# Performance work log

Hardware: AMD Instinct MI355X
Metric: run time of the kernel (lower is better)

## Reference

```python
import jax, jax.numpy as jnp
import numpy as np

N, E, F, H, OUT, PROP_STEPS, NUM_LAYERS = 50000, 800000, 64, 128, 32, 3, 2


def setup_inputs() -> dict:
    key = jax.random.key(0)
    ks = jax.random.split(key, 24)
    def lin(kw, kb, out_d, in_d):
        s = 1.0 / np.sqrt(in_d)
        w = jax.random.uniform(kw, (out_d, in_d), jnp.float32, -s, s)
        b = jax.random.uniform(kb, (out_d,), jnp.float32, -s, s)
        return w, b
    enc_w, enc_b = lin(ks[0], ks[1], 1, 2)
    ratt_w, ratt_b = lin(ks[2], ks[3], 1, F)
    iatt_w, iatt_b = lin(ks[4], ks[5], 1, F)
    rlin0_w, rlin0_b = lin(ks[6], ks[7], H, F)
    rlin1_w, rlin1_b = lin(ks[8], ks[9], H, H)
    ilin0_w, ilin0_b = lin(ks[10], ks[11], H, F)
    ilin1_w, ilin1_b = lin(ks[12], ks[13], H, H)
    out_w, out_b = lin(ks[14], ks[15], OUT, 2 * H)
    return {
        'real_feature': jax.random.normal(ks[16], (N, F), jnp.float32),
        'imag_feature': jax.random.normal(ks[17], (N, F), jnp.float32),
        'edge_entropy': jax.random.uniform(ks[18], (E,), jnp.float32),
        'edge_cluster_coefficient': jax.random.uniform(ks[19], (E,), jnp.float32),
        'edge_weight_sym': jax.random.uniform(ks[20], (E,), jnp.float32),
        'exp_weight_q': jnp.asarray(0.5, jnp.float32),
        'enc_w': enc_w, 'enc_b': enc_b,
        'ratt_w': ratt_w, 'ratt_b': ratt_b,
        'iatt_w': iatt_w, 'iatt_b': iatt_b,
        'rlin0_w': rlin0_w, 'rlin0_b': rlin0_b,
        'rlin1_w': rlin1_w, 'rlin1_b': rlin1_b,
        'ilin0_w': ilin0_w, 'ilin0_b': ilin0_b,
        'ilin1_w': ilin1_w, 'ilin1_b': ilin1_b,
        'out_w': out_w, 'out_b': out_b,
        'row': jax.random.randint(ks[21], (E,), 0, N, jnp.int32),
        'col': jax.random.randint(ks[22], (E,), 0, N, jnp.int32),
    }


def reference(real_feature, imag_feature, edge_entropy, edge_cluster_coefficient,
              edge_weight_sym, exp_weight_q, enc_w, enc_b, ratt_w, ratt_b,
              iatt_w, iatt_b, rlin0_w, rlin0_b, rlin1_w, rlin1_b,
              ilin0_w, ilin0_b, ilin1_w, ilin1_b, out_w, out_b, row, col):
    n = real_feature.shape[0]
    # structural encoding -> complex phase per edge (soft_label is None branch)
    structure_info = jnp.stack((edge_entropy, edge_cluster_coefficient), axis=1)  # [E,2]
    se = (structure_info @ enc_w.T + enc_b).reshape(-1)                            # [E]
    phase = exp_weight_q * se
    wr = edge_weight_sym * jnp.cos(phase)  # real adj values
    wi = edge_weight_sym * jnp.sin(phase)  # imag adj values

    reals, imags = [real_feature], [imag_feature]
    for _ in range(PROP_STEPS):
        xr = reals[-1][col]  # [E,F] gather once, shared by both SpMMs
        xi = imags[-1][col]
        # complex SpMM: (wr + i*wi) * (xr + i*xi)
        msg_r = wr[:, None] * xr - wi[:, None] * xi
        msg_i = wi[:, None] * xr + wr[:, None] * xi
        reals.append(jax.ops.segment_sum(msg_r, row, num_segments=n))
        imags.append(jax.ops.segment_sum(msg_i, row, num_segments=n))

    R = jnp.stack(reals)  # [S+1, N, F]
    I = jnp.stack(imags)

    # attention pooling over prop steps (softmax over step axis, per node)
    ra = R @ ratt_w.T + ratt_b  # [S+1, N, 1]
    ia = I @ iatt_w.T + iatt_b
    rw = jax.nn.softmax(jax.nn.sigmoid(ra[..., 0]), axis=0)  # [S+1, N]
    iw = jax.nn.softmax(jax.nn.sigmoid(ia[..., 0]), axis=0)
    real_x = jnp.einsum('snf,sn->nf', R, rw)
    imag_x = jnp.einsum('snf,sn->nf', I, iw)

    # complex MLP with ComReLU (mask both parts by sign of real part); dropout=0 -> identity
    for (rw_, rb_, iw_, ib_) in ((rlin0_w, rlin0_b, ilin0_w, ilin0_b),
                                 (rlin1_w, rlin1_b, ilin1_w, ilin1_b)):
        zr = real_x @ rw_.T + rb_
        zi = imag_x @ iw_.T + ib_
        mask = (zr >= 0).astype(zr.dtype)
        real_x, imag_x = zr * mask, zi * mask

    x = jnp.concatenate((real_x, imag_x), axis=-1)
    return x @ out_w.T + out_b
```

## Files before the change

kernel.cpp:

```cpp
#include <hip/hip_runtime.h>

#define N_NODES 50000
#define N_EDGES 800000
#define FDIM 64
#define NST 50000
#define SA_BLOCKS ((N_NODES + 1023) / 1024)


__global__ __launch_bounds__(256) void hist_kernel(const int* __restrict__ row,
                                                   int* __restrict__ cnt, int E) {
  int e = blockIdx.x * 256 + threadIdx.x;
  if (e < E) atomicAdd(&cnt[row[e]], 1);
}

__global__ __launch_bounds__(1024) void scanA_kernel(const int* __restrict__ cnt,
                                                     int* __restrict__ offs,
                                                     int* __restrict__ bsum,
                                                     int n) {
  __shared__ int s[1024];
  int t = threadIdx.x;
  int i = blockIdx.x * 1024 + t;
  int v = (i < n) ? cnt[i] : 0;
  s[t] = v;
  __syncthreads();
  for (int d = 1; d < 1024; d <<= 1) {
    int add = (t >= d) ? s[t - d] : 0;
    __syncthreads();
    s[t] += add;
    __syncthreads();
  }
  if (i < n) offs[i] = s[t] - v;
  if (t == 1023) bsum[blockIdx.x] = s[1023];
}

__global__ __launch_bounds__(64) void scanB_kernel(int* __restrict__ bsum,
                                                   int* __restrict__ boff,
                                                   int nb) {
  __shared__ int s[64];
  int t = threadIdx.x;
  int v = (t < nb) ? bsum[t] : 0;
  s[t] = v;
  __syncthreads();
  for (int d = 1; d < 64; d <<= 1) {
    int add = (t >= d) ? s[t - d] : 0;
    __syncthreads();
    s[t] += add;
    __syncthreads();
  }
  if (t < nb) boff[t] = s[t] - v;
}

__global__ __launch_bounds__(1024) void scanC_kernel(int* __restrict__ offs,
                                                     int* __restrict__ cursor,
                                                     const int* __restrict__ boff,
                                                     int n, int E) {
  int t = threadIdx.x;
  int i = blockIdx.x * 1024 + t;
  int bo = boff[blockIdx.x];
  if (i < n) {
    int o = offs[i] + bo;
    offs[i] = o;
    cursor[i] = o;
  }
  if (i == 0) offs[n] = E;
}

__global__ __launch_bounds__(256) void scatter_kernel(
    const int* __restrict__ row, const int* __restrict__ col,
    const float* __restrict__ ent, const float* __restrict__ ccf,
    const float* __restrict__ wsym, const float* __restrict__ encw,
    const float* __restrict__ encb, const float* __restrict__ q,
    int* __restrict__ cursor, int* __restrict__ col_s,
    float2* __restrict__ ws, int E) {
  int e = blockIdx.x * 256 + threadIdx.x;
  if (e >= E) return;
  float se = encw[0] * ent[e] + encw[1] * ccf[e] + encb[0];
  float ph = q[0] * se;
  float sw, cw;
  sincosf(ph, &sw, &cw);
  float w = wsym[e];
  int pos = atomicAdd(&cursor[row[e]], 1);
  col_s[pos] = col[e];
  ws[pos] = make_float2(w * cw, w * sw);
}


__global__ __launch_bounds__(256) void prep_weights(
    const float* __restrict__ r0, const float* __restrict__ i0,
    const float* __restrict__ r1, const float* __restrict__ i1,
    float* __restrict__ r0T, float* __restrict__ i0T, float* __restrict__ r1T,
    float* __restrict__ i1T) {
  int t = blockIdx.x * 256 + threadIdx.x;
  if (t < 128 * 64) {
    int h = t / 64, f = t % 64;
    r0T[f * 128 + h] = r0[t];
    i0T[f * 128 + h] = i0[t];
  }
  if (t < 128 * 128) {
    int h = t / 128, f = t % 128;
    r1T[f * 128 + h] = r1[t];
    i1T[f * 128 + h] = i1[t];
  }
}


__global__ __launch_bounds__(256) void pack_kernel(const float* __restrict__ re,
                                                   const float* __restrict__ im,
                                                   float2* __restrict__ X,
                                                   int total) {
  int i = blockIdx.x * 256 + threadIdx.x;
  if (i < total) X[i] = make_float2(re[i], im[i]);
}


__global__ __launch_bounds__(256) void prop_kernel(
    const float* __restrict__ X, float* __restrict__ Y,
    const int* __restrict__ offs, const int* __restrict__ col_s,
    const float2* __restrict__ ws, int n) {
  int wave = (int)((blockIdx.x * (size_t)blockDim.x + threadIdx.x) >> 6);
  int lane = threadIdx.x & 63;
  if (wave >= n) return;
  int half = lane >> 5, l5 = lane & 31;
  const float* Xl = X + l5 * 4;
  int beg = offs[wave], end = offs[wave + 1];
  float4 acc = make_float4(0.f, 0.f, 0.f, 0.f);
  int j = beg;
  for (; j + 16 <= end; j += 16) {
    int c[8];
    float2 w[8];
    float4 x[8];
#pragma unroll
    for (int k = 0; k < 8; ++k) c[k] = col_s[j + 2 * k + half];
#pragma unroll
    for (int k = 0; k < 8; ++k) w[k] = ws[j + 2 * k + half];
#pragma unroll
    for (int k = 0; k < 8; ++k) x[k] = *(const float4*)&Xl[(size_t)c[k] * 128];
#pragma unroll
    for (int k = 0; k < 8; ++k) {
      acc.x += w[k].x * x[k].x - w[k].y * x[k].y;
      acc.y += w[k].y * x[k].x + w[k].x * x[k].y;
      acc.z += w[k].x * x[k].z - w[k].y * x[k].w;
      acc.w += w[k].y * x[k].z + w[k].x * x[k].w;
    }
  }
  for (; j + 8 <= end; j += 8) {
    int c[4];
    float2 w[4];
    float4 x[4];
#pragma unroll
    for (int k = 0; k < 4; ++k) c[k] = col_s[j + 2 * k + half];
#pragma unroll
    for (int k = 0; k < 4; ++k) w[k] = ws[j + 2 * k + half];
#pragma unroll
    for (int k = 0; k < 4; ++k) x[k] = *(const float4*)&Xl[(size_t)c[k] * 128];
#pragma unroll
    for (int k = 0; k < 4; ++k) {
      acc.x += w[k].x * x[k].x - w[k].y * x[k].y;
      acc.y += w[k].y * x[k].x + w[k].x * x[k].y;
      acc.z += w[k].x * x[k].z - w[k].y * x[k].w;
      acc.w += w[k].y * x[k].z + w[k].x * x[k].w;
    }
  }
  for (; j + 4 <= end; j += 4) {
    int c0 = col_s[j + half];
    int c1 = col_s[j + 2 + half];
    float2 w0 = ws[j + half];
    float2 w1 = ws[j + 2 + half];
    float4 x0 = *(const float4*)&Xl[(size_t)c0 * 128];
    float4 x1 = *(const float4*)&Xl[(size_t)c1 * 128];
    acc.x += w0.x * x0.x - w0.y * x0.y;
    acc.y += w0.y * x0.x + w0.x * x0.y;
    acc.z += w0.x * x0.z - w0.y * x0.w;
    acc.w += w0.y * x0.z + w0.x * x0.w;
    acc.x += w1.x * x1.x - w1.y * x1.y;
    acc.y += w1.y * x1.x + w1.x * x1.y;
    acc.z += w1.x * x1.z - w1.y * x1.w;
    acc.w += w1.y * x1.z + w1.x * x1.w;
  }
  for (; j < end; j += 2) {
    int je = j + half;
    bool valid = je < end;
    int jc = valid ? je : beg;
    float2 w = ws[jc];
    float wr = valid ? w.x : 0.f;
    float wi = valid ? w.y : 0.f;
    int cc = col_s[jc];
    float4 x = *(const float4*)&Xl[(size_t)cc * 128];
    acc.x += wr * x.x - wi * x.y;
    acc.y += wi * x.x + wr * x.y;
    acc.z += wr * x.z - wi * x.w;
    acc.w += wi * x.z + wr * x.w;
  }
  acc.x += __shfl_xor(acc.x, 32, 64);
  acc.y += __shfl_xor(acc.y, 32, 64);
  acc.z += __shfl_xor(acc.z, 32, 64);
  acc.w += __shfl_xor(acc.w, 32, 64);
  if (lane < 32) *(float4*)&Y[(size_t)wave * 128 + l5 * 4] = acc;
}


__device__ __forceinline__ float wave_sum(float v) {
#pragma unroll
  for (int d = 32; d > 0; d >>= 1) v += __shfl_xor(v, d, 64);
  return v;
}

__global__ __launch_bounds__(256) void pool_kernel(
    const float* __restrict__ R0f, const float* __restrict__ I0f,
    const float* __restrict__ X1, const float* __restrict__ X2,
    const float* __restrict__ X3, const float* __restrict__ rattw,
    const float* __restrict__ rattb, const float* __restrict__ iattw,
    const float* __restrict__ iattb, float* __restrict__ PT, int n) {
  __shared__ float pt[128 * 65];
  int wid = threadIdx.x >> 6, lane = threadIdx.x & 63;
  int nb = blockIdx.x * 64;
  float aw = rattw[lane], bw = iattw[lane];
  float rb0 = rattb[0], ib0 = iattb[0];
  for (int k = 0; k < 16; ++k) {
    int ln = wid * 16 + k;
    int nc = min(nb + ln, n - 1);
    float r0 = R0f[(size_t)nc * 64 + lane];
    float q0 = I0f[(size_t)nc * 64 + lane];
    size_t base = (size_t)nc * 128 + 2 * lane;
    float2 v1 = *(const float2*)&X1[base];
    float2 v2 = *(const float2*)&X2[base];
    float2 v3 = *(const float2*)&X3[base];
    float ra0 = wave_sum(r0 * aw) + rb0;
    float ra1 = wave_sum(v1.x * aw) + rb0;
    float ra2 = wave_sum(v2.x * aw) + rb0;
    float ra3 = wave_sum(v3.x * aw) + rb0;
    float ia0 = wave_sum(q0 * bw) + ib0;
    float ia1 = wave_sum(v1.y * bw) + ib0;
    float ia2 = wave_sum(v2.y * bw) + ib0;
    float ia3 = wave_sum(v3.y * bw) + ib0;
    float s0 = 1.f / (1.f + __expf(-ra0));
    float s1 = 1.f / (1.f + __expf(-ra1));
    float s2 = 1.f / (1.f + __expf(-ra2));
    float s3 = 1.f / (1.f + __expf(-ra3));
    float t0 = 1.f / (1.f + __expf(-ia0));
    float t1 = 1.f / (1.f + __expf(-ia1));
    float t2 = 1.f / (1.f + __expf(-ia2));
    float t3 = 1.f / (1.f + __expf(-ia3));
    float mR = fmaxf(fmaxf(s0, s1), fmaxf(s2, s3));
    float e0 = __expf(s0 - mR), e1 = __expf(s1 - mR), e2 = __expf(s2 - mR),
          e3 = __expf(s3 - mR);
    float invR = 1.f / (e0 + e1 + e2 + e3);
    float mI = fmaxf(fmaxf(t0, t1), fmaxf(t2, t3));
    float g0 = __expf(t0 - mI), g1 = __expf(t1 - mI), g2 = __expf(t2 - mI),
          g3 = __expf(t3 - mI);
    float invI = 1.f / (g0 + g1 + g2 + g3);
    float pr = (r0 * e0 + v1.x * e1 + v2.x * e2 + v3.x * e3) * invR;
    float pi = (q0 * g0 + v1.y * g1 + v2.y * g2 + v3.y * g3) * invI;
    pt[lane * 65 + ln] = pr;
    pt[(64 + lane) * 65 + ln] = pi;
  }
  __syncthreads();
  int c = threadIdx.x & 63, fr = threadIdx.x >> 6;
  for (int r = 0; r < 32; ++r) {
    int f = fr * 32 + r;
    int nd = nb + c;
    if (nd < n) PT[(size_t)f * NST + nd] = pt[f * 65 + c];
  }
}


__global__ __launch_bounds__(512, 8) void mlp_kernel(
    const float* __restrict__ PT, const float* __restrict__ r0T,
    const float* __restrict__ r0b, const float* __restrict__ i0T,
    const float* __restrict__ i0b, const float* __restrict__ r1T,
    const float* __restrict__ r1b, const float* __restrict__ i1T,
    const float* __restrict__ i1b, const float* __restrict__ ow,
    const float* __restrict__ ob, float* __restrict__ out, int n) {
  __shared__ float zt[128 * 65];
  int lane = threadIdx.x & 63;
  int wid = threadIdx.x >> 6;
  int h0 = __builtin_amdgcn_readfirstlane(wid * 16);
  int nb = blockIdx.x * 64;
  int node = min(nb + lane, n - 1);

  float zr[16], zi[16];
#pragma unroll
  for (int j = 0; j < 16; ++j) {
    zr[j] = r0b[h0 + j];
    zi[j] = i0b[h0 + j];
  }
#pragma unroll 2
  for (int f = 0; f < 64; ++f) {
    float ar = PT[(size_t)f * NST + node];
    float ai = PT[(size_t)(64 + f) * NST + node];
    const float* wr = &r0T[f * 128 + h0];
    const float* wi = &i0T[f * 128 + h0];
#pragma unroll
    for (int j = 0; j < 16; ++j) {
      zr[j] += ar * wr[j];
      zi[j] += ai * wi[j];
    }
  }
#pragma unroll
  for (int j = 0; j < 16; ++j) {
    float m = (zr[j] >= 0.f) ? 1.f : 0.f;
    zr[j] *= m;
    zi[j] *= m;
  }

#pragma unroll
  for (int j = 0; j < 16; ++j) zt[(h0 + j) * 65 + lane] = zr[j];
  __syncthreads();
  float yr[16];
#pragma unroll
  for (int j = 0; j < 16; ++j) yr[j] = r1b[h0 + j];
#pragma unroll 2
  for (int f = 0; f < 128; ++f) {
    float a = zt[f * 65 + lane];
    const float* w = &r1T[f * 128 + h0];
#pragma unroll
    for (int j = 0; j < 16; ++j) yr[j] += a * w[j];
  }
  __syncthreads();

#pragma unroll
  for (int j = 0; j < 16; ++j) zt[(h0 + j) * 65 + lane] = zi[j];
  __syncthreads();
  float yi[16];
#pragma unroll
  for (int j = 0; j < 16; ++j) yi[j] = i1b[h0 + j];
#pragma unroll 2
  for (int f = 0; f < 128; ++f) {
    float a = zt[f * 65 + lane];
    const float* w = &i1T[f * 128 + h0];
#pragma unroll
    for (int j = 0; j < 16; ++j) yi[j] += a * w[j];
  }
#pragma unroll
  for (int j = 0; j < 16; ++j) {
    float m = (yr[j] >= 0.f) ? 1.f : 0.f;
    yr[j] *= m;
    yi[j] *= m;
  }
  __syncthreads();

  int o0 = __builtin_amdgcn_readfirstlane(wid * 4);
  float os[4] = {0.f, 0.f, 0.f, 0.f};
#pragma unroll
  for (int j = 0; j < 16; ++j) zt[(h0 + j) * 65 + lane] = yr[j];
  __syncthreads();
#pragma unroll 2
  for (int h = 0; h < 128; ++h) {
    float v = zt[h * 65 + lane];
    const float* w = &ow[o0 * 256 + h];
#pragma unroll
    for (int oo = 0; oo < 4; ++oo) os[oo] += v * w[oo * 256];
  }
  __syncthreads();
#pragma unroll
  for (int j = 0; j < 16; ++j) zt[(h0 + j) * 65 + lane] = yi[j];
  __syncthreads();
#pragma unroll 2
  for (int h = 0; h < 128; ++h) {
    float v = zt[h * 65 + lane];
    const float* w = &ow[o0 * 256 + 128 + h];
#pragma unroll
    for (int oo = 0; oo < 4; ++oo) os[oo] += v * w[oo * 256];
  }
#pragma unroll
  for (int oo = 0; oo < 4; ++oo)
    out[(size_t)node * 32 + o0 + oo] = os[oo] + ob[o0 + oo];
}


extern "C" void kernel_launch(void* const* d_in, const int* in_sizes, int n_in,
                              void* d_out, int out_size, void* d_ws,
                              size_t ws_size, hipStream_t stream) {
  const float* realf = (const float*)d_in[0];
  const float* imagf = (const float*)d_in[1];
  const float* ent = (const float*)d_in[2];
  const float* ccf = (const float*)d_in[3];
  const float* wsym = (const float*)d_in[4];
  const float* q = (const float*)d_in[5];
  const float* encw = (const float*)d_in[6];
  const float* encb = (const float*)d_in[7];
  const float* rattw = (const float*)d_in[8];
  const float* rattb = (const float*)d_in[9];
  const float* iattw = (const float*)d_in[10];
  const float* iattb = (const float*)d_in[11];
  const float* r0w = (const float*)d_in[12];
  const float* r0b = (const float*)d_in[13];
  const float* r1w = (const float*)d_in[14];
  const float* r1b = (const float*)d_in[15];
  const float* i0w = (const float*)d_in[16];
  const float* i0b = (const float*)d_in[17];
  const float* i1w = (const float*)d_in[18];
  const float* i1b = (const float*)d_in[19];
  const float* ow = (const float*)d_in[20];
  const float* ob = (const float*)d_in[21];
  const int* row = (const int*)d_in[22];
  const int* col = (const int*)d_in[23];
  float* out = (float*)d_out;

  char* p = (char*)d_ws;
  auto alloc = [&](size_t bytes) -> void* {
    void* r = (void*)p;
    p += (bytes + 255) & ~(size_t)255;
    return r;
  };
  int* cnt = (int*)alloc(N_NODES * sizeof(int));
  int* offs = (int*)alloc((N_NODES + 1) * sizeof(int));
  int* bsum = (int*)alloc(SA_BLOCKS * sizeof(int));
  int* boff = (int*)alloc(SA_BLOCKS * sizeof(int));
  int* col_s = (int*)alloc(N_EDGES * sizeof(int));
  float2* ws2 = (float2*)alloc(N_EDGES * sizeof(float2));
  size_t NX = (size_t)N_NODES * 128 * sizeof(float);
  float* X0 = (float*)alloc(NX);
  float* X1 = (float*)alloc(NX);
  float* X2 = (float*)alloc(NX);
  float* X3 = (float*)alloc(NX);
  float* PT = (float*)alloc((size_t)128 * NST * sizeof(float));
  float* r0T = (float*)alloc(64 * 128 * 4);
  float* i0T = (float*)alloc(64 * 128 * 4);
  float* r1T = (float*)alloc(128 * 128 * 4);
  float* i1T = (float*)alloc(128 * 128 * 4);

  hipMemsetAsync(cnt, 0, N_NODES * sizeof(int), stream);
  prep_weights<<<64, 256, 0, stream>>>(r0w, i0w, r1w, i1w, r0T, i0T, r1T, i1T);
  hist_kernel<<<(N_EDGES + 255) / 256, 256, 0, stream>>>(row, cnt, N_EDGES);
  scanA_kernel<<<SA_BLOCKS, 1024, 0, stream>>>(cnt, offs, bsum, N_NODES);
  scanB_kernel<<<1, 64, 0, stream>>>(bsum, boff, SA_BLOCKS);
  scanC_kernel<<<SA_BLOCKS, 1024, 0, stream>>>(offs, cnt, boff, N_NODES,
                                               N_EDGES);
  scatter_kernel<<<(N_EDGES + 255) / 256, 256, 0, stream>>>(
      row, col, ent, ccf, wsym, encw, encb, q, cnt, col_s, ws2, N_EDGES);
  pack_kernel<<<(N_NODES * 64 + 255) / 256, 256, 0, stream>>>(
      realf, imagf, (float2*)X0, N_NODES * 64);

  const int pgrid = (N_NODES + 3) / 4;
  prop_kernel<<<pgrid, 256, 0, stream>>>(X0, X1, offs, col_s, ws2, N_NODES);
  prop_kernel<<<pgrid, 256, 0, stream>>>(X1, X2, offs, col_s, ws2, N_NODES);
  prop_kernel<<<pgrid, 256, 0, stream>>>(X2, X3, offs, col_s, ws2, N_NODES);

  const int hgrid = (N_NODES + 63) / 64;
  pool_kernel<<<hgrid, 256, 0, stream>>>(realf, imagf, X1, X2, X3, rattw,
                                         rattb, iattw, iattb, PT, N_NODES);
  mlp_kernel<<<hgrid, 512, 0, stream>>>(PT, r0T, r0b, i0T, i0b, r1T, r1b, i1T,
                                        i1b, ow, ob, out, N_NODES);
}
```

Baseline: 423.7 us.

## Use full-wave float2 gathers in propagation and row-major float4 LDS tiles in MLP

```diff
diff --git a/kernel.cpp b/kernel.cpp
--- a/kernel.cpp
+++ b/kernel.cpp
@@ -120,82 +120,44 @@
   int wave = (int)((blockIdx.x * (size_t)blockDim.x + threadIdx.x) >> 6);
   int lane = threadIdx.x & 63;
   if (wave >= n) return;
-  int half = lane >> 5, l5 = lane & 31;
-  const float* Xl = X + l5 * 4;
-  int beg = offs[wave], end = offs[wave + 1];
-  float4 acc = make_float4(0.f, 0.f, 0.f, 0.f);
+  int beg = __builtin_amdgcn_readfirstlane(offs[wave]);
+  int end = __builtin_amdgcn_readfirstlane(offs[wave + 1]);
+  const float2* Xl = (const float2*)X + lane;
+  float2 acc = make_float2(0.f, 0.f);
   int j = beg;
-  for (; j + 16 <= end; j += 16) {
+  for (; j + 8 <= end; j += 8) {
     int c[8];
-    float2 w[8];
-    float4 x[8];
-#pragma unroll
-    for (int k = 0; k < 8; ++k) c[k] = col_s[j + 2 * k + half];
-#pragma unroll
-    for (int k = 0; k < 8; ++k) w[k] = ws[j + 2 * k + half];
-#pragma unroll
-    for (int k = 0; k < 8; ++k) x[k] = *(const float4*)&Xl[(size_t)c[k] * 128];
+#pragma unroll
+    for (int k = 0; k < 8; ++k) c[k] = col_s[j + k];
+    float2 x[8];
+#pragma unroll
+    for (int k = 0; k < 8; ++k) x[k] = Xl[(size_t)c[k] * 64];
 #pragma unroll
     for (int k = 0; k < 8; ++k) {
-      acc.x += w[k].x * x[k].x - w[k].y * x[k].y;
-      acc.y += w[k].y * x[k].x + w[k].x * x[k].y;
-      acc.z += w[k].x * x[k].z - w[k].y * x[k].w;
-      acc.w += w[k].y * x[k].z + w[k].x * x[k].w;
+      float2 w = ws[j + k];
+      acc.x += w.x * x[k].x - w.y * x[k].y;
+      acc.y += w.y * x[k].x + w.x * x[k].y;
     }
   }
-  for (; j + 8 <= end; j += 8) {
-    int c[4];
-    float2 w[4];
-    float4 x[4];
-#pragma unroll
-    for (int k = 0; k < 4; ++k) c[k] = col_s[j + 2 * k + half];
-#pragma unroll
-    for (int k = 0; k < 4; ++k) w[k] = ws[j + 2 * k + half];
-#pragma unroll
-    for (int k = 0; k < 4; ++k) x[k] = *(const float4*)&Xl[(size_t)c[k] * 128];
-#pragma unroll
-    for (int k = 0; k < 4; ++k) {
-      acc.x += w[k].x * x[k].x - w[k].y * x[k].y;
-      acc.y += w[k].y * x[k].x + w[k].x * x[k].y;
-      acc.z += w[k].x * x[k].z - w[k].y * x[k].w;
-      acc.w += w[k].y * x[k].z + w[k].x * x[k].w;
-    }
-  }
-  for (; j + 4 <= end; j += 4) {
-    int c0 = col_s[j + half];
-    int c1 = col_s[j + 2 + half];
-    float2 w0 = ws[j + half];
-    float2 w1 = ws[j + 2 + half];
-    float4 x0 = *(const float4*)&Xl[(size_t)c0 * 128];
-    float4 x1 = *(const float4*)&Xl[(size_t)c1 * 128];
-    acc.x += w0.x * x0.x - w0.y * x0.y;
-    acc.y += w0.y * x0.x + w0.x * x0.y;
-    acc.z += w0.x * x0.z - w0.y * x0.w;
-    acc.w += w0.y * x0.z + w0.x * x0.w;
-    acc.x += w1.x * x1.x - w1.y * x1.y;
-    acc.y += w1.y * x1.x + w1.x * x1.y;
-    acc.z += w1.x * x1.z - w1.y * x1.w;
-    acc.w += w1.y * x1.z + w1.x * x1.w;
-  }
-  for (; j < end; j += 2) {
-    int je = j + half;
-    bool valid = je < end;
-    int jc = valid ? je : beg;
-    float2 w = ws[jc];
-    float wr = valid ? w.x : 0.f;
-    float wi = valid ? w.y : 0.f;
-    int cc = col_s[jc];
-    float4 x = *(const float4*)&Xl[(size_t)cc * 128];
-    acc.x += wr * x.x - wi * x.y;
-    acc.y += wi * x.x + wr * x.y;
-    acc.z += wr * x.z - wi * x.w;
-    acc.w += wi * x.z + wr * x.w;
-  }
-  acc.x += __shfl_xor(acc.x, 32, 64);
-  acc.y += __shfl_xor(acc.y, 32, 64);
-  acc.z += __shfl_xor(acc.z, 32, 64);
-  acc.w += __shfl_xor(acc.w, 32, 64);
-  if (lane < 32) *(float4*)&Y[(size_t)wave * 128 + l5 * 4] = acc;
+  int rem = end - j;
+  if (rem > 0) {
+    int c[8];
+#pragma unroll
+    for (int k = 0; k < 8; ++k)
+      if (k < rem) c[k] = col_s[j + k];
+    float2 x[8];
+#pragma unroll
+    for (int k = 0; k < 8; ++k)
+      if (k < rem) x[k] = Xl[(size_t)c[k] * 64];
+#pragma unroll
+    for (int k = 0; k < 8; ++k)
+      if (k < rem) {
+        float2 w = ws[j + k];
+        acc.x += w.x * x[k].x - w.y * x[k].y;
+        acc.y += w.y * x[k].x + w.x * x[k].y;
+      }
+  }
+  ((float2*)Y)[(size_t)wave * 64 + lane] = acc;
 }
 
 
@@ -271,12 +233,13 @@
     const float* __restrict__ r1b, const float* __restrict__ i1T,
     const float* __restrict__ i1b, const float* __restrict__ ow,
     const float* __restrict__ ob, float* __restrict__ out, int n) {
-  __shared__ float zt[128 * 65];
+  __shared__ float zt[64 * 132];
   int lane = threadIdx.x & 63;
   int wid = threadIdx.x >> 6;
   int h0 = __builtin_amdgcn_readfirstlane(wid * 16);
   int nb = blockIdx.x * 64;
   int node = min(nb + lane, n - 1);
+  float* zrow = &zt[lane * 132];
 
   float zr[16], zi[16];
 #pragma unroll
@@ -304,32 +267,44 @@
   }
 
 #pragma unroll
-  for (int j = 0; j < 16; ++j) zt[(h0 + j) * 65 + lane] = zr[j];
+  for (int j4 = 0; j4 < 4; ++j4)
+    *(float4*)&zrow[h0 + 4 * j4] = make_float4(zr[4 * j4], zr[4 * j4 + 1],
+                                               zr[4 * j4 + 2], zr[4 * j4 + 3]);
   __syncthreads();
   float yr[16];
 #pragma unroll
   for (int j = 0; j < 16; ++j) yr[j] = r1b[h0 + j];
 #pragma unroll 2
-  for (int f = 0; f < 128; ++f) {
-    float a = zt[f * 65 + lane];
-    const float* w = &r1T[f * 128 + h0];
-#pragma unroll
-    for (int j = 0; j < 16; ++j) yr[j] += a * w[j];
-  }
-  __syncthreads();
-
-#pragma unroll
-  for (int j = 0; j < 16; ++j) zt[(h0 + j) * 65 + lane] = zi[j];
+  for (int f4 = 0; f4 < 32; ++f4) {
+    float4 a4 = *(const float4*)&zrow[4 * f4];
+    const float* w0 = &r1T[(4 * f4) * 128 + h0];
+    const float* w1 = &r1T[(4 * f4 + 1) * 128 + h0];
+    const float* w2 = &r1T[(4 * f4 + 2) * 128 + h0];
+    const float* w3 = &r1T[(4 * f4 + 3) * 128 + h0];
+#pragma unroll
+    for (int j = 0; j < 16; ++j)
+      yr[j] += a4.x * w0[j] + a4.y * w1[j] + a4.z * w2[j] + a4.w * w3[j];
+  }
+  __syncthreads();
+
+#pragma unroll
+  for (int j4 = 0; j4 < 4; ++j4)
+    *(float4*)&zrow[h0 + 4 * j4] = make_float4(zi[4 * j4], zi[4 * j4 + 1],
+                                               zi[4 * j4 + 2], zi[4 * j4 + 3]);
   __syncthreads();
   float yi[16];
 #pragma unroll
   for (int j = 0; j < 16; ++j) yi[j] = i1b[h0 + j];
 #pragma unroll 2
-  for (int f = 0; f < 128; ++f) {
-    float a = zt[f * 65 + lane];
-    const float* w = &i1T[f * 128 + h0];
-#pragma unroll
-    for (int j = 0; j < 16; ++j) yi[j] += a * w[j];
+  for (int f4 = 0; f4 < 32; ++f4) {
+    float4 a4 = *(const float4*)&zrow[4 * f4];
+    const float* w0 = &i1T[(4 * f4) * 128 + h0];
+    const float* w1 = &i1T[(4 * f4 + 1) * 128 + h0];
+    const float* w2 = &i1T[(4 * f4 + 2) * 128 + h0];
+    const float* w3 = &i1T[(4 * f4 + 3) * 128 + h0];
+#pragma unroll
+    for (int j = 0; j < 16; ++j)
+      yi[j] += a4.x * w0[j] + a4.y * w1[j] + a4.z * w2[j] + a4.w * w3[j];
   }
 #pragma unroll
   for (int j = 0; j < 16; ++j) {
@@ -342,25 +317,33 @@
   int o0 = __builtin_amdgcn_readfirstlane(wid * 4);
   float os[4] = {0.f, 0.f, 0.f, 0.f};
 #pragma unroll
-  for (int j = 0; j < 16; ++j) zt[(h0 + j) * 65 + lane] = yr[j];
+  for (int j4 = 0; j4 < 4; ++j4)
+    *(float4*)&zrow[h0 + 4 * j4] = make_float4(yr[4 * j4], yr[4 * j4 + 1],
+                                               yr[4 * j4 + 2], yr[4 * j4 + 3]);
   __syncthreads();
 #pragma unroll 2
-  for (int h = 0; h < 128; ++h) {
-    float v = zt[h * 65 + lane];
-    const float* w = &ow[o0 * 256 + h];
-#pragma unroll
-    for (int oo = 0; oo < 4; ++oo) os[oo] += v * w[oo * 256];
-  }
-  __syncthreads();
-#pragma unroll
-  for (int j = 0; j < 16; ++j) zt[(h0 + j) * 65 + lane] = yi[j];
+  for (int f4 = 0; f4 < 32; ++f4) {
+    float4 v = *(const float4*)&zrow[4 * f4];
+#pragma unroll
+    for (int oo = 0; oo < 4; ++oo) {
+      const float* w = &ow[(o0 + oo) * 256 + 4 * f4];
+      os[oo] += v.x * w[0] + v.y * w[1] + v.z * w[2] + v.w * w[3];
+    }
+  }
+  __syncthreads();
+#pragma unroll
+  for (int j4 = 0; j4 < 4; ++j4)
+    *(float4*)&zrow[h0 + 4 * j4] = make_float4(yi[4 * j4], yi[4 * j4 + 1],
+                                               yi[4 * j4 + 2], yi[4 * j4 + 3]);
   __syncthreads();
 #pragma unroll 2
-  for (int h = 0; h < 128; ++h) {
-    float v = zt[h * 65 + lane];
-    const float* w = &ow[o0 * 256 + 128 + h];
-#pragma unroll
-    for (int oo = 0; oo < 4; ++oo) os[oo] += v * w[oo * 256];
+  for (int f4 = 0; f4 < 32; ++f4) {
+    float4 v = *(const float4*)&zrow[4 * f4];
+#pragma unroll
+    for (int oo = 0; oo < 4; ++oo) {
+      const float* w = &ow[(o0 + oo) * 256 + 128 + 4 * f4];
+      os[oo] += v.x * w[0] + v.y * w[1] + v.z * w[2] + v.w * w[3];
+    }
   }
 #pragma unroll
   for (int oo = 0; oo < 4; ++oo)
```

Result: no change. 425.3 us (+0.4%).
